# Kernel optimization log

Hardware: AMD Instinct MI355X
Metric: run time of the kernel (lower is better)

## Reference

```python
import jax, jax.numpy as jnp
import numpy as np

MODEL_DIM = 1024
NUM_HEADS = 16
HEAD_DIM = MODEL_DIM // NUM_HEADS
B, L = 2, 2048


def setup_inputs() -> dict:
    key = jax.random.key(0)
    ks = jax.random.split(key, 11)
    s = 1.0 / np.sqrt(MODEL_DIM)
    inp = {
        "q": jax.random.normal(ks[0], (B, L, MODEL_DIM), jnp.float32),
        "k": jax.random.normal(ks[1], (B, L, MODEL_DIM), jnp.float32),
        "v": jax.random.normal(ks[2], (B, L, MODEL_DIM), jnp.float32),
        "Wq": jax.random.uniform(ks[3], (MODEL_DIM, MODEL_DIM), jnp.float32, -s, s),
        "bq": jax.random.uniform(ks[4], (MODEL_DIM,), jnp.float32, -s, s),
        "Wk": jax.random.uniform(ks[5], (MODEL_DIM, MODEL_DIM), jnp.float32, -s, s),
        "bk": jax.random.uniform(ks[6], (MODEL_DIM,), jnp.float32, -s, s),
        "Wv": jax.random.uniform(ks[7], (MODEL_DIM, MODEL_DIM), jnp.float32, -s, s),
        "bv": jax.random.uniform(ks[8], (MODEL_DIM,), jnp.float32, -s, s),
        "Wo": jax.random.uniform(ks[9], (MODEL_DIM, MODEL_DIM), jnp.float32, -s, s),
        "bo": jax.random.uniform(ks[10], (MODEL_DIM,), jnp.float32, -s, s),
    }
    return inp


def reference(q, k, v, Wq, bq, Wk, bk, Wv, bv, Wo, bo):
    Bq, Lq, D = q.shape
    H, Hd = NUM_HEADS, HEAD_DIM
    # Linear projections (torch Linear: x @ W.T + b)
    Q = q @ Wq.T + bq
    K = k @ Wk.T + bk
    V = v @ Wv.T + bv
    # split heads -> [B, H, L, Hd]
    def split(x):
        return x.reshape(Bq, Lq, H, Hd).transpose(0, 2, 1, 3)
    Qh, Kh, Vh = split(Q), split(K), split(V)
    scale = 1.0 / jnp.sqrt(jnp.asarray(Hd, Q.dtype))
    scores = jnp.einsum("bhqd,bhkd->bhqk", Qh, Kh) * scale
    attn = jax.nn.softmax(scores, axis=-1)  # dropout = identity in eval
    ctx = jnp.einsum("bhqk,bhkd->bhqd", attn, Vh)
    ctx = ctx.transpose(0, 2, 1, 3).reshape(Bq, Lq, D)
    return ctx @ Wo.T + bo
```

## Files before the change

### kernel.cpp

```cpp
#include <hip/hip_runtime.h>


typedef __attribute__((ext_vector_type(4))) float f32x4;
typedef __attribute__((ext_vector_type(16))) float f32x16;
typedef __attribute__((ext_vector_type(4))) unsigned int u32x4;
typedef __attribute__((ext_vector_type(2))) unsigned int u32x2;
typedef __attribute__((ext_vector_type(8))) short bf16x8;

#define DEVI static __device__ __forceinline__

DEVI unsigned short f2bf(float x) {
  union { float f; unsigned u; } v; v.f = x;
  unsigned r = v.u + 0x7fffu + ((v.u >> 16) & 1u);
  return (unsigned short)(r >> 16);
}

DEVI unsigned cvtpk(float lo, float hi) {
  unsigned r;
  asm("v_cvt_pk_bf16_f32 %0, %1, %2" : "=v"(r) : "v"(lo), "v"(hi));
  return r;
}

DEVI float exp2v(float x) {
  float y;
  asm("v_exp_f32 %0, %1" : "=v"(y) : "v"(x));
  return y;
}

DEVI void gload_lds16(const void* g, void* l) {
  __builtin_amdgcn_global_load_lds((__attribute__((address_space(1))) void*)g,
                                   (__attribute__((address_space(3))) void*)l, 16, 0, 0);
}

#define WAIT_VM(N) asm volatile("s_waitcnt vmcnt(" #N ")" ::: "memory")
#define BARRIER __builtin_amdgcn_s_barrier()

constexpr int MD = 1024;
constexpr int NH = 16;
constexpr int HD = 64;
constexpr int LL = 2048;
constexpr float CQ = 0.18033688011112042f;
constexpr float CREF = 8.0f;

struct CvtArgs { const float* src[7]; unsigned short* dst[7]; };

__global__ void cvt_kernel(CvtArgs a) {
  const int bx = blockIdx.x;
  int which, base;
  if (bx < 2048) { which = bx >> 9;            base = (bx & 511) * 2048; }
  else           { which = 4 + ((bx - 2048) >> 11); base = ((bx - 2048) & 2047) * 2048; }
  const float* w = a.src[which];
  unsigned short* o = a.dst[which];
  const int i = base + threadIdx.x * 8;
  f32x4 x = *(const f32x4*)(w + i);
  f32x4 y = *(const f32x4*)(w + i + 4);
  union { unsigned u[4]; u32x4 q; } r;
  r.u[0] = cvtpk(x[0], x[1]); r.u[1] = cvtpk(x[2], x[3]);
  r.u[2] = cvtpk(y[0], y[1]); r.u[3] = cvtpk(y[2], y[3]);
  *(u32x4*)(o + i) = r.q;
}

struct QKVArgs {
  const unsigned short* A[3];
  const unsigned short* W[3];
  const float* bias[3];
  unsigned short* out[3];
};

__global__ __launch_bounds__(256, 3) void gemm_qkv(QKVArgs args) {
  __shared__ alignas(16) unsigned short Abuf[3][128 * 32];
  __shared__ alignas(16) unsigned short Bbuf[3][128 * 32];

  const int tid = threadIdx.x;
  const int lane = tid & 63;
  const int wave = tid >> 6;
  const int wr = wave >> 1, wc = wave & 1;
  const int lr = lane & 15, lg = lane >> 4;

  const int logical = (int)(blockIdx.x & 7) * 96 + (int)(blockIdx.x >> 3);
  const int n0 = (logical & 7) * 128;
  const int y = logical >> 3;
  const int mode = y >> 5;
  const int m0 = (y & 31) * 128;

  const unsigned short* Ab = args.A[mode];
  const unsigned short* Wb = args.W[mode];
  const float* bias = args.bias[mode];
  unsigned short* Out = args.out[mode];

  const int rrow = lane >> 2, rslot = lane & 3;

  f32x4 acc[4][4] = {};

  auto stage = [&](int slot, int kt) {
    const int k0 = kt * 32;
    #pragma unroll
    for (int sh = 0; sh < 2; ++sh) {
      const int row = sh * 64 + wave * 16 + rrow;
      const int ss = rslot ^ ((row >> 1) & 3);
      gload_lds16((const char*)(Ab + (size_t)(m0 + row) * 1024 + k0) + ss * 16,
                  (char*)&Abuf[slot][0] + sh * 4096 + wave * 1024);
    }
    #pragma unroll
    for (int sh = 0; sh < 2; ++sh) {
      const int row = sh * 64 + wave * 16 + rrow;
      const int ss = rslot ^ ((row >> 1) & 3);
      gload_lds16((const char*)(Wb + (size_t)(n0 + row) * 1024 + k0) + ss * 16,
                  (char*)&Bbuf[slot][0] + sh * 4096 + wave * 1024);
    }
  };

  stage(0, 0); stage(1, 1);

  int slot = 0;
  for (int kt = 0; kt < 32; ++kt) {
    if (kt < 31) WAIT_VM(4);
    else         WAIT_VM(0);
    BARRIER;
    if (kt < 30) stage((slot + 2 >= 3) ? slot - 1 : slot + 2, kt + 2);

    bf16x8 af[4], bfr[4];
    #pragma unroll
    for (int mi = 0; mi < 4; ++mi) {
      const int row = wr * 64 + mi * 16 + lr;
      af[mi] = *(const bf16x8*)((const char*)&Abuf[slot][0] + row * 64 +
                                (((unsigned)lg ^ ((row >> 1) & 3)) << 4));
    }
    #pragma unroll
    for (int ni = 0; ni < 4; ++ni) {
      const int row = wc * 64 + ni * 16 + lr;
      bfr[ni] = *(const bf16x8*)((const char*)&Bbuf[slot][0] + row * 64 +
                                 (((unsigned)lg ^ ((row >> 1) & 3)) << 4));
    }
    __builtin_amdgcn_s_setprio(1);
    #pragma unroll
    for (int mi = 0; mi < 4; ++mi)
      #pragma unroll
      for (int ni = 0; ni < 4; ++ni)
        acc[mi][ni] = __builtin_amdgcn_mfma_f32_16x16x32_bf16(af[mi], bfr[ni], acc[mi][ni], 0, 0, 0);
    __builtin_amdgcn_s_setprio(0);

    slot = (slot + 1 >= 3) ? 0 : slot + 1;
  }

  float bv[4];
  const int cn = n0 + wc * 64 + lr;
  #pragma unroll
  for (int ni = 0; ni < 4; ++ni) bv[ni] = bias[cn + ni * 16];

  #pragma unroll
  for (int mi = 0; mi < 4; ++mi) {
    #pragma unroll
    for (int j = 0; j < 4; ++j) {
      const int m = m0 + wr * 64 + mi * 16 + lg * 4 + j;
      const int b = m >> 11, l = m & 2047;
      #pragma unroll
      for (int ni = 0; ni < 4; ++ni) {
        const int n = cn + ni * 16;
        const int h = n >> 6, d = n & 63;
        float val = acc[mi][ni][j] + bv[ni];
        if (mode == 0) val *= CQ;
        if (mode == 2)
          Out[((size_t)(b * NH + h) * HD + d) * LL + l] = f2bf(val);
        else
          Out[((size_t)(b * NH + h) * LL + l) * HD + d] = f2bf(val);
      }
    }
  }
}

__global__ __launch_bounds__(256, 3) void gemm_out(const unsigned short* __restrict__ Ab,
                                                   const unsigned short* __restrict__ Wb,
                                                   const float* __restrict__ bias,
                                                   float* __restrict__ Out) {
  __shared__ alignas(16) unsigned short Abuf[3][128 * 32];
  __shared__ alignas(16) unsigned short Bbuf[3][128 * 32];

  const int tid = threadIdx.x;
  const int lane = tid & 63;
  const int wave = tid >> 6;
  const int wr = wave >> 1, wc = wave & 1;
  const int lr = lane & 15, lg = lane >> 4;

  const int logical = (int)(blockIdx.x & 7) * 32 + (int)(blockIdx.x >> 3);
  const int n0 = (logical & 7) * 128;
  const int m0 = (logical >> 3) * 128;

  const int rrow = lane >> 2, rslot = lane & 3;

  f32x4 acc[4][4] = {};

  auto stage = [&](int slot, int kt) {
    const int k0 = kt * 32;
    #pragma unroll
    for (int sh = 0; sh < 2; ++sh) {
      const int row = sh * 64 + wave * 16 + rrow;
      const int ss = rslot ^ ((row >> 1) & 3);
      gload_lds16((const char*)(Ab + (size_t)(m0 + row) * 1024 + k0) + ss * 16,
                  (char*)&Abuf[slot][0] + sh * 4096 + wave * 1024);
    }
    #pragma unroll
    for (int sh = 0; sh < 2; ++sh) {
      const int row = sh * 64 + wave * 16 + rrow;
      const int ss = rslot ^ ((row >> 1) & 3);
      gload_lds16((const char*)(Wb + (size_t)(n0 + row) * 1024 + k0) + ss * 16,
                  (char*)&Bbuf[slot][0] + sh * 4096 + wave * 1024);
    }
  };

  stage(0, 0); stage(1, 1);

  int slot = 0;
  for (int kt = 0; kt < 32; ++kt) {
    if (kt < 31) WAIT_VM(4);
    else         WAIT_VM(0);
    BARRIER;
    if (kt < 30) stage((slot + 2 >= 3) ? slot - 1 : slot + 2, kt + 2);

    bf16x8 af[4], bfr[4];
    #pragma unroll
    for (int mi = 0; mi < 4; ++mi) {
      const int row = wr * 64 + mi * 16 + lr;
      af[mi] = *(const bf16x8*)((const char*)&Abuf[slot][0] + row * 64 +
                                (((unsigned)lg ^ ((row >> 1) & 3)) << 4));
    }
    #pragma unroll
    for (int ni = 0; ni < 4; ++ni) {
      const int row = wc * 64 + ni * 16 + lr;
      bfr[ni] = *(const bf16x8*)((const char*)&Bbuf[slot][0] + row * 64 +
                                 (((unsigned)lg ^ ((row >> 1) & 3)) << 4));
    }
    __builtin_amdgcn_s_setprio(1);
    #pragma unroll
    for (int mi = 0; mi < 4; ++mi)
      #pragma unroll
      for (int ni = 0; ni < 4; ++ni)
        acc[mi][ni] = __builtin_amdgcn_mfma_f32_16x16x32_bf16(af[mi], bfr[ni], acc[mi][ni], 0, 0, 0);
    __builtin_amdgcn_s_setprio(0);

    slot = (slot + 1 >= 3) ? 0 : slot + 1;
  }

  float bv[4];
  const int cn = n0 + wc * 64 + lr;
  #pragma unroll
  for (int ni = 0; ni < 4; ++ni) bv[ni] = bias[cn + ni * 16];

  #pragma unroll
  for (int mi = 0; mi < 4; ++mi)
    #pragma unroll
    for (int j = 0; j < 4; ++j) {
      const int m = m0 + wr * 64 + mi * 16 + lg * 4 + j;
      #pragma unroll
      for (int ni = 0; ni < 4; ++ni)
        Out[(size_t)m * 1024 + cn + ni * 16] = acc[mi][ni][j] + bv[ni];
    }
}

__global__ __launch_bounds__(256, 2) void attn_kernel(const unsigned short* __restrict__ Qh,
                                                      const unsigned short* __restrict__ Kh,
                                                      const unsigned short* __restrict__ Vt,
                                                      unsigned short* __restrict__ Ctx) {
  constexpr int KB = 64;
  constexpr int NT = LL / KB;
  __shared__ alignas(16) unsigned short Kl[3][KB * HD];
  __shared__ alignas(16) unsigned short Vl[3][HD * KB];

  const int tid = threadIdx.x;
  const int lane = tid & 63;
  const int wave = tid >> 6;
  const int lq = lane & 31;
  const int hi = lane >> 5;

  const int logical = (int)(blockIdx.x & 7) * 64 + (int)(blockIdx.x >> 3);
  const int bh = logical >> 4;
  const int q0 = (logical & 15) * 128 + wave * 32;

  const unsigned short* Kg = Kh + (size_t)bh * LL * HD;
  const unsigned short* Vg = Vt + (size_t)bh * HD * LL;

  bf16x8 qf[4];
  {
    const unsigned short* qp = Qh + (size_t)bh * LL * HD + (size_t)(q0 + lq) * HD + hi * 8;
    #pragma unroll
    for (int s = 0; s < 4; ++s) qf[s] = *(const bf16x8*)(qp + s * 16);
  }

  f32x16 oacc0 = {}, oacc1 = {};
  float s_ = 0.f;

  auto stage = [&](int slot, int t) {
    #pragma unroll
    for (int shot = 0; shot < 2; ++shot) {
      const int o = shot * 4096 + tid * 16;
      const int row = o >> 7, col = o & 127;
      const int sc = col ^ ((row & 7) << 4);
      gload_lds16((const char*)Kg + (size_t)(t * KB + row) * (HD * 2) + sc,
                  (char*)&Kl[slot][0] + shot * 4096 + wave * 1024);
    }
    #pragma unroll
    for (int shot = 0; shot < 2; ++shot) {
      const int o = shot * 4096 + tid * 16;
      const int row = o >> 7, col = o & 127;
      const int sc = col ^ ((row & 7) << 4);
      gload_lds16((const char*)Vg + (size_t)row * (LL * 2) + t * (KB * 2) + sc,
                  (char*)&Vl[slot][0] + shot * 4096 + wave * 1024);
    }
  };

  stage(0, 0); stage(1, 1);

  int slot = 0;
  for (int t = 0; t < NT; ++t) {
    if (t < NT - 1) WAIT_VM(4);
    else            WAIT_VM(0);
    BARRIER;
    if (t < NT - 2) stage((slot + 2 >= 3) ? slot - 1 : slot + 2, t + 2);

    const int swz = (lq & 7) << 4;

    bf16x8 kf0[4], kf1[4], vf0[4], vf1[4];
    #pragma unroll
    for (int s = 0; s < 4; ++s) {
      const int off = ((s * 32 + hi * 16) ^ swz);
      kf0[s] = *(const bf16x8*)((const char*)&Kl[slot][0] + lq * 128 + off);
      kf1[s] = *(const bf16x8*)((const char*)&Kl[slot][0] + (32 + lq) * 128 + off);
    }
    #pragma unroll
    for (int s = 0; s < 4; ++s) {
      const int off = ((s * 32 + hi * 16) ^ swz);
      vf0[s] = *(const bf16x8*)((const char*)&Vl[slot][0] + lq * 128 + off);
      vf1[s] = *(const bf16x8*)((const char*)&Vl[slot][0] + (32 + lq) * 128 + off);
    }

    f32x16 st0 = {}, st1 = {};
    __builtin_amdgcn_s_setprio(1);
    #pragma unroll
    for (int s = 0; s < 4; ++s) {
      st0 = __builtin_amdgcn_mfma_f32_32x32x16_bf16(kf0[s], qf[s], st0, 0, 0, 0);
      st1 = __builtin_amdgcn_mfma_f32_32x32x16_bf16(kf1[s], qf[s], st1, 0, 0, 0);
    }
    __builtin_amdgcn_s_setprio(0);

    float a4[4] = {0.f, 0.f, 0.f, 0.f};
    #pragma unroll
    for (int i = 0; i < 16; ++i) {
      float y0 = exp2v(st0[i] - CREF);
      float y1 = exp2v(st1[i] - CREF);
      st0[i] = y0; st1[i] = y1;
      a4[i & 3] += y0; a4[i & 3] += y1;
    }
    s_ += (a4[0] + a4[1]) + (a4[2] + a4[3]);

    bf16x8 pfr[4];
    #pragma unroll
    for (int s = 0; s < 4; ++s) {
      const int r = (s & 1) * 8;
      float p0, p1, p2, p3, p4, p5, p6, p7;
      if (s < 2) {
        p0 = st0[r+0]; p1 = st0[r+1]; p2 = st0[r+2]; p3 = st0[r+3];
        p4 = st0[r+4]; p5 = st0[r+5]; p6 = st0[r+6]; p7 = st0[r+7];
      } else {
        p0 = st1[r+0]; p1 = st1[r+1]; p2 = st1[r+2]; p3 = st1[r+3];
        p4 = st1[r+4]; p5 = st1[r+5]; p6 = st1[r+6]; p7 = st1[r+7];
      }
      unsigned a0 = cvtpk(p0, p1);
      unsigned a1 = cvtpk(p2, p3);
      unsigned a2 = cvtpk(p4, p5);
      unsigned a3 = cvtpk(p6, p7);
      asm volatile("v_permlane32_swap_b32 %0, %1" : "+v"(a0), "+v"(a2));
      asm volatile("v_permlane32_swap_b32 %0, %1" : "+v"(a1), "+v"(a3));
      union { unsigned u[4]; bf16x8 v; } pf;
      pf.u[0] = a0;
      pf.u[1] = a1;
      pf.u[2] = a2;
      pf.u[3] = a3;
      pfr[s] = pf.v;
    }

    __builtin_amdgcn_s_setprio(1);
    #pragma unroll
    for (int s = 0; s < 4; ++s) {
      oacc0 = __builtin_amdgcn_mfma_f32_32x32x16_bf16(vf0[s], pfr[s], oacc0, 0, 0, 0);
      oacc1 = __builtin_amdgcn_mfma_f32_32x32x16_bf16(vf1[s], pfr[s], oacc1, 0, 0, 0);
    }
    __builtin_amdgcn_s_setprio(0);

    slot = (slot + 1 >= 3) ? 0 : slot + 1;
  }

  s_ += __shfl_xor(s_, 32);
  const float inv = 1.0f / s_;
  const int b = bh >> 4, h = bh & 15;
  const int q = q0 + lq;
  unsigned short* op = Ctx + ((size_t)(b * LL + q)) * MD + h * HD;
  #pragma unroll
  for (int g = 0; g < 4; ++g) {
    {
      union { unsigned short us[4]; u32x2 u; } w;
      #pragma unroll
      for (int j = 0; j < 4; ++j) w.us[j] = f2bf(oacc0[g * 4 + j] * inv);
      *(u32x2*)(op + 8 * g + 4 * hi) = w.u;
    }
    {
      union { unsigned short us[4]; u32x2 u; } w;
      #pragma unroll
      for (int j = 0; j < 4; ++j) w.us[j] = f2bf(oacc1[g * 4 + j] * inv);
      *(u32x2*)(op + 32 + 8 * g + 4 * hi) = w.u;
    }
  }
}

extern "C" void kernel_launch(void* const* d_in, const int* in_sizes, int n_in,
                              void* d_out, int out_size, void* d_ws, size_t ws_size,
                              hipStream_t stream) {
  const float* q  = (const float*)d_in[0];
  const float* k  = (const float*)d_in[1];
  const float* v  = (const float*)d_in[2];
  const float* Wq = (const float*)d_in[3];
  const float* bq = (const float*)d_in[4];
  const float* Wk = (const float*)d_in[5];
  const float* bk = (const float*)d_in[6];
  const float* Wv = (const float*)d_in[7];
  const float* bv = (const float*)d_in[8];
  const float* Wo = (const float*)d_in[9];
  const float* bo = (const float*)d_in[10];

  char* ws = (char*)d_ws;
  const size_t MB = 1u << 20;
  unsigned short* Wqb = (unsigned short*)(ws + 0 * MB);
  unsigned short* Wkb = (unsigned short*)(ws + 2 * MB);
  unsigned short* Wvb = (unsigned short*)(ws + 4 * MB);
  unsigned short* Wob = (unsigned short*)(ws + 6 * MB);
  unsigned short* Qhb = (unsigned short*)(ws + 8 * MB);
  unsigned short* Khb = (unsigned short*)(ws + 16 * MB);
  unsigned short* Vtb = (unsigned short*)(ws + 24 * MB);
  unsigned short* ctx = (unsigned short*)(ws + 32 * MB);
  unsigned short* qb  = (unsigned short*)(ws + 40 * MB);
  unsigned short* kb  = (unsigned short*)(ws + 48 * MB);
  unsigned short* vb  = (unsigned short*)(ws + 56 * MB);

  CvtArgs ca;
  ca.src[0] = Wq; ca.src[1] = Wk; ca.src[2] = Wv; ca.src[3] = Wo;
  ca.src[4] = q;  ca.src[5] = k;  ca.src[6] = v;
  ca.dst[0] = Wqb; ca.dst[1] = Wkb; ca.dst[2] = Wvb; ca.dst[3] = Wob;
  ca.dst[4] = qb;  ca.dst[5] = kb;  ca.dst[6] = vb;
  cvt_kernel<<<8192, 256, 0, stream>>>(ca);

  QKVArgs args;
  args.A[0] = qb;  args.A[1] = kb;  args.A[2] = vb;
  args.W[0] = Wqb; args.W[1] = Wkb; args.W[2] = Wvb;
  args.bias[0] = bq; args.bias[1] = bk; args.bias[2] = bv;
  args.out[0] = Qhb; args.out[1] = Khb; args.out[2] = Vtb;
  gemm_qkv<<<768, 256, 0, stream>>>(args);

  attn_kernel<<<512, 256, 0, stream>>>(Qhb, Khb, Vtb, ctx);

  gemm_out<<<256, 256, 0, stream>>>(ctx, Wob, bo, (float*)d_out);
}
```

Baseline: 136.1 us.

## Enlarge QKV GEMM tiles to 256x256x64 with 512-thread blocks and double buffering

Reworks the fused QKV projection GEMM from 128x128x32 tiles on 256 threads with a 3-slot pipeline to 256x256x64 tiles on 512 threads (8 waves, each computing a 128x64 sub-tile) with 2-slot double buffering and a new 8-way XOR swizzle. The larger tile raises arithmetic intensity and reduces global and LDS traffic per FLOP. In exchange, the grid shrinks from 768 to 192 blocks, which is fewer than the CU count, so load balance and occupancy may suffer. Prefetch depth also drops to one stage with a full vmcnt(0) wait each iteration.

```diff
diff --git a/kernel.cpp b/kernel.cpp
--- a/kernel.cpp
+++ b/kernel.cpp
@@ -67,98 +67,98 @@
   unsigned short* out[3];
 };
 
-__global__ __launch_bounds__(256, 3) void gemm_qkv(QKVArgs args) {
-  __shared__ alignas(16) unsigned short Abuf[3][128 * 32];
-  __shared__ alignas(16) unsigned short Bbuf[3][128 * 32];
+__global__ __launch_bounds__(512, 2) void gemm_qkv(QKVArgs args) {
+  __shared__ alignas(16) unsigned short Abuf[2][256 * 64];
+  __shared__ alignas(16) unsigned short Bbuf[2][256 * 64];
 
   const int tid = threadIdx.x;
   const int lane = tid & 63;
   const int wave = tid >> 6;
-  const int wr = wave >> 1, wc = wave & 1;
+  const int wm = wave >> 2, wn = wave & 3;
   const int lr = lane & 15, lg = lane >> 4;
 
-  const int logical = (int)(blockIdx.x & 7) * 96 + (int)(blockIdx.x >> 3);
-  const int n0 = (logical & 7) * 128;
-  const int y = logical >> 3;
-  const int mode = y >> 5;
-  const int m0 = (y & 31) * 128;
+  const int logical = (int)(blockIdx.x & 7) * 24 + (int)(blockIdx.x >> 3);
+  const int mode = logical >> 6;
+  const int rem = logical & 63;
+  const int m0 = (rem >> 2) * 256;
+  const int n0 = (rem & 3) * 256;
 
   const unsigned short* Ab = args.A[mode];
   const unsigned short* Wb = args.W[mode];
   const float* bias = args.bias[mode];
   unsigned short* Out = args.out[mode];
 
-  const int rrow = lane >> 2, rslot = lane & 3;
-
-  f32x4 acc[4][4] = {};
-
-  auto stage = [&](int slot, int kt) {
-    const int k0 = kt * 32;
-    #pragma unroll
-    for (int sh = 0; sh < 2; ++sh) {
-      const int row = sh * 64 + wave * 16 + rrow;
-      const int ss = rslot ^ ((row >> 1) & 3);
+  f32x4 acc[8][4] = {};
+
+  auto stage = [&](int buf, int kt) {
+    const int k0 = kt * 64;
+    #pragma unroll
+    for (int sh = 0; sh < 4; ++sh) {
+      const int row = sh * 64 + (tid >> 3);
+      const int ss = (tid & 7) ^ (row & 7);
       gload_lds16((const char*)(Ab + (size_t)(m0 + row) * 1024 + k0) + ss * 16,
-                  (char*)&Abuf[slot][0] + sh * 4096 + wave * 1024);
-    }
-    #pragma unroll
-    for (int sh = 0; sh < 2; ++sh) {
-      const int row = sh * 64 + wave * 16 + rrow;
-      const int ss = rslot ^ ((row >> 1) & 3);
+                  (char*)&Abuf[buf][0] + sh * 8192 + wave * 1024);
+    }
+    #pragma unroll
+    for (int sh = 0; sh < 4; ++sh) {
+      const int row = sh * 64 + (tid >> 3);
+      const int ss = (tid & 7) ^ (row & 7);
       gload_lds16((const char*)(Wb + (size_t)(n0 + row) * 1024 + k0) + ss * 16,
-                  (char*)&Bbuf[slot][0] + sh * 4096 + wave * 1024);
+                  (char*)&Bbuf[buf][0] + sh * 8192 + wave * 1024);
     }
   };
 
-  stage(0, 0); stage(1, 1);
-
-  int slot = 0;
-  for (int kt = 0; kt < 32; ++kt) {
-    if (kt < 31) WAIT_VM(4);
-    else         WAIT_VM(0);
+  stage(0, 0);
+
+  for (int kt = 0; kt < 16; ++kt) {
+    const int buf = kt & 1;
+    WAIT_VM(0);
     BARRIER;
-    if (kt < 30) stage((slot + 2 >= 3) ? slot - 1 : slot + 2, kt + 2);
-
-    bf16x8 af[4], bfr[4];
-    #pragma unroll
-    for (int mi = 0; mi < 4; ++mi) {
-      const int row = wr * 64 + mi * 16 + lr;
-      af[mi] = *(const bf16x8*)((const char*)&Abuf[slot][0] + row * 64 +
-                                (((unsigned)lg ^ ((row >> 1) & 3)) << 4));
-    }
-    #pragma unroll
-    for (int ni = 0; ni < 4; ++ni) {
-      const int row = wc * 64 + ni * 16 + lr;
-      bfr[ni] = *(const bf16x8*)((const char*)&Bbuf[slot][0] + row * 64 +
-                                 (((unsigned)lg ^ ((row >> 1) & 3)) << 4));
-    }
-    __builtin_amdgcn_s_setprio(1);
-    #pragma unroll
-    for (int mi = 0; mi < 4; ++mi)
-      #pragma unroll
-      for (int ni = 0; ni < 4; ++ni)
-        acc[mi][ni] = __builtin_amdgcn_mfma_f32_16x16x32_bf16(af[mi], bfr[ni], acc[mi][ni], 0, 0, 0);
-    __builtin_amdgcn_s_setprio(0);
-
-    slot = (slot + 1 >= 3) ? 0 : slot + 1;
+    if (kt < 15) stage(buf ^ 1, kt + 1);
+
+    bf16x8 bfr[2][4];
+    #pragma unroll
+    for (int ks = 0; ks < 2; ++ks)
+      #pragma unroll
+      for (int nf = 0; nf < 4; ++nf) {
+        const int row = wn * 64 + nf * 16 + lr;
+        bfr[ks][nf] = *(const bf16x8*)((const char*)&Bbuf[buf][0] + row * 128 +
+                       ((unsigned)((ks * 4 + lg) ^ (row & 7)) << 4));
+      }
+
+    #pragma unroll
+    for (int mf = 0; mf < 8; ++mf) {
+      const int row = wm * 128 + mf * 16 + lr;
+      const char* base = (const char*)&Abuf[buf][0] + row * 128;
+      bf16x8 a0 = *(const bf16x8*)(base + ((unsigned)((0 + lg) ^ (row & 7)) << 4));
+      bf16x8 a1 = *(const bf16x8*)(base + ((unsigned)((4 + lg) ^ (row & 7)) << 4));
+      __builtin_amdgcn_s_setprio(1);
+      #pragma unroll
+      for (int nf = 0; nf < 4; ++nf)
+        acc[mf][nf] = __builtin_amdgcn_mfma_f32_16x16x32_bf16(a0, bfr[0][nf], acc[mf][nf], 0, 0, 0);
+      #pragma unroll
+      for (int nf = 0; nf < 4; ++nf)
+        acc[mf][nf] = __builtin_amdgcn_mfma_f32_16x16x32_bf16(a1, bfr[1][nf], acc[mf][nf], 0, 0, 0);
+      __builtin_amdgcn_s_setprio(0);
+    }
   }
 
   float bv[4];
-  const int cn = n0 + wc * 64 + lr;
+  const int cn = n0 + wn * 64 + lr;
   #pragma unroll
-  for (int ni = 0; ni < 4; ++ni) bv[ni] = bias[cn + ni * 16];
+  for (int nf = 0; nf < 4; ++nf) bv[nf] = bias[cn + nf * 16];
 
   #pragma unroll
-  for (int mi = 0; mi < 4; ++mi) {
+  for (int mf = 0; mf < 8; ++mf) {
     #pragma unroll
     for (int j = 0; j < 4; ++j) {
-      const int m = m0 + wr * 64 + mi * 16 + lg * 4 + j;
+      const int m = m0 + wm * 128 + mf * 16 + lg * 4 + j;
       const int b = m >> 11, l = m & 2047;
       #pragma unroll
-      for (int ni = 0; ni < 4; ++ni) {
-        const int n = cn + ni * 16;
+      for (int nf = 0; nf < 4; ++nf) {
+        const int n = cn + nf * 16;
         const int h = n >> 6, d = n & 63;
-        float val = acc[mi][ni][j] + bv[ni];
+        float val = acc[mf][nf][j] + bv[nf];
         if (mode == 0) val *= CQ;
         if (mode == 2)
           Out[((size_t)(b * NH + h) * HD + d) * LL + l] = f2bf(val);
@@ -452,7 +452,7 @@
   args.W[0] = Wqb; args.W[1] = Wkb; args.W[2] = Wvb;
   args.bias[0] = bq; args.bias[1] = bk; args.bias[2] = bv;
   args.out[0] = Qhb; args.out[1] = Khb; args.out[2] = Vtb;
-  gemm_qkv<<<768, 256, 0, stream>>>(args);
+  gemm_qkv<<<192, 512, 0, stream>>>(args);
 
   attn_kernel<<<512, 256, 0, stream>>>(Qhb, Khb, Vtb, ctx);
 
```

Result: slower. 145.2 us (+6.7%).
